# Optimization experiments

Hardware: AMD Instinct MI355X
Metric: run time of the kernel (lower is better)

Reference implementation:

```python
import jax, jax.numpy as jnp
import numpy as np

B, D, K, DM = 4096, 64, 64, 512  # batch, latent_dim, num_charts, d_model
BALL_EPS = 1e-5


def _l2n(x):
    return x / (jnp.linalg.norm(x) + 1e-12)


def _spectral_scale(W, iters=5):
    # torch.nn.utils.spectral_norm semantics: power iteration with no-grad u,v,
    # gradient flows through W in sigma = u^T W v.
    Wd = jax.lax.stop_gradient(W)
    u = _l2n(jnp.ones((W.shape[0],), W.dtype))
    v = _l2n(Wd.T @ u)
    for _ in range(iters):
        v = _l2n(Wd.T @ u)
        u = _l2n(Wd @ v)
    sigma = u @ (W @ v)
    return W / sigma


def spectral_linear(x, W, b):
    return x @ _spectral_scale(W).T + b


def _project_to_ball(x):
    n = jnp.linalg.norm(x, axis=-1, keepdims=True)
    scale = jnp.minimum(1.0, (1.0 - BALL_EPS) / jnp.maximum(n, 1e-12))
    return x * scale


def _poincare_dist2(x, y):
    # x: [B, D] query positions, y: [B, K, D] chart centers -> squared geodesic dist [B, K]
    diff2 = jnp.sum((x[:, None, :] - y) ** 2, axis=-1)
    den = (1.0 - jnp.sum(x * x, axis=-1, keepdims=True)) * (1.0 - jnp.sum(y * y, axis=-1))
    arg = 1.0 + 2.0 * diff2 / jnp.maximum(den, 1e-12)
    d = jnp.arccosh(jnp.maximum(arg, 1.0 + 1e-7))
    return d * d


def covariant_attention(z_q, z_kv, x_q, x_k, x_v, Wq, bq, Wk, bk, Wv, bv, Wo, bo, geo_scale):
    # Single-head geodesic-biased attention (GeodesicConfig n_heads=1).
    q = x_q @ Wq.T + bq                               # [B, DM]
    k = jnp.einsum('bkd,ed->bke', x_k, Wk) + bk       # [B, K, DM]
    v = jnp.einsum('bkd,ed->bke', x_v, Wv) + bv       # [B, K, DM]
    scores = jnp.einsum('bd,bkd->bk', q, k) / jnp.sqrt(jnp.asarray(DM, q.dtype))
    scores = scores - geo_scale * _poincare_dist2(z_q, z_kv)
    attn = jax.nn.softmax(scores, axis=-1)            # [B, K]
    feat = jnp.einsum('bk,bkd->bd', attn, v)
    out = feat @ Wo.T + bo                            # [B, DM]
    return out, attn


def setup_inputs() -> dict:
    keys = jax.random.split(jax.random.key(0), 20)
    z = 0.05 * jax.random.normal(keys[0], (B, D), jnp.float32)      # inside unit ball
    rw = jax.nn.softmax(jax.random.normal(keys[1], (B, K), jnp.float32), axis=-1)
    chart_emb = 0.02 * jax.random.normal(keys[2], (K, DM), jnp.float32)
    cc = jax.random.normal(keys[3], (K, D), jnp.float32)
    chart_centers = 0.3 * (cc / jnp.linalg.norm(cc, axis=-1, keepdims=True))
    s = 0.02
    return {
        'z': z, 'rw': rw,
        'chart_emb': chart_emb, 'chart_centers': chart_centers,
        'zW': s * jax.random.normal(keys[4], (DM, D), jnp.float32),
        'zb': jnp.zeros((DM,), jnp.float32),
        'Wq': s * jax.random.normal(keys[5], (DM, DM), jnp.float32),
        'bq': jnp.zeros((DM,), jnp.float32),
        'Wk': s * jax.random.normal(keys[6], (DM, DM), jnp.float32),
        'bk': jnp.zeros((DM,), jnp.float32),
        'Wv': s * jax.random.normal(keys[7], (DM, DM), jnp.float32),
        'bv': jnp.zeros((DM,), jnp.float32),
        'Wo': s * jax.random.normal(keys[8], (DM, DM), jnp.float32),
        'bo': jnp.zeros((DM,), jnp.float32),
        'geo_scale': jnp.ones((), jnp.float32),
        'vW': s * jax.random.normal(keys[9], (1, DM), jnp.float32),
        'vb': jnp.zeros((1,), jnp.float32),
    }


def reference(z, rw, chart_emb, chart_centers, zW, zb, Wq, bq, Wk, bk, Wv, bv, Wo, bo, geo_scale, vW, vb):
    # ChartTokenizer: broadcast-multiply router weights with chart embeddings
    tokens_x = rw[:, :, None] * chart_emb[None]            # [B, K, DM]
    tokens_z = jnp.broadcast_to(_project_to_ball(chart_centers)[None], (z.shape[0], K, D))
    # z embedding (SpectralLinear)
    x_q = spectral_linear(z, zW, zb)                       # [B, DM]
    # critic covariant attention
    v_feat, _ = covariant_attention(z, tokens_z, x_q, tokens_x, tokens_x,
                                    Wq, bq, Wk, bk, Wv, bv, Wo, bo, geo_scale)
    # task value head (SpectralLinear -> scalar)
    return spectral_linear(v_feat, vW, vb)                 # [B, 1]
```

## Files before the change

### kernel.cpp

```cpp
#include <hip/hip_runtime.h>
#include <math.h>

#define WS_INV    0
#define WS_INVSV  1
#define WS_BOVW   2
#define WS_BVWO   3
#define WS_N2V    4
#define WS_COLSUM 64
#define WS_A      128
#define WS_WO0    4224
#define WS_QZB    4736
#define WS_CK0    5248
#define WS_CVW    5312
#define WS_NY2    5376
#define WS_YT     5440
#define WS_T1     16384
#define WS_V1     49152
#define WS_P1     81920
#define WS_GP     114688

#define PRE_LDSB  (36928 * 4)
#define MID_LDSB  (8192 * 4)
#define MAIN_LDSB (8448 * 4)

__device__ __forceinline__ float wave_sum(float x) {
#pragma unroll
    for (int o = 32; o; o >>= 1) x += __shfl_xor(x, o);
    return x;
}

__device__ __forceinline__ float block_sum512(float v, float* red) {
    float s = wave_sum(v);
    const int wid = threadIdx.x >> 6;
    __syncthreads();
    if ((threadIdx.x & 63) == 0) red[wid] = s;
    __syncthreads();
    float t2 = 0.0f;
#pragma unroll
    for (int i = 0; i < 8; ++i) t2 += red[i];
    return t2;
}

__global__ __launch_bounds__(512) void k_pre(
    const float* __restrict__ zW, const float* __restrict__ zb,
    const float* __restrict__ Wq, const float* __restrict__ bq,
    const float* __restrict__ Wk, const float* __restrict__ Wv,
    const float* __restrict__ Wo, const float* __restrict__ ce,
    const float* __restrict__ cc, const float* __restrict__ vW,
    const float* __restrict__ bo, float* __restrict__ ws)
{
    extern __shared__ float sm[];
    const int blk = blockIdx.x, t = threadIdx.x;
    const int lane = t & 63, w = t >> 6;

    if (blk < 128) {
        const int f0 = blk * 4;
        float* ces = sm;
        float* wkv = sm + 32832;
        {
            const float4* ce4 = (const float4*)ce;
#pragma unroll 4
            for (int i = 0; i < 16; ++i) {
                const int idx4 = i * 512 + t;
                const int k = idx4 >> 7, c4 = idx4 & 127;
                const float4 v = ce4[idx4];
                float* dst = &ces[k * 513 + c4 * 4];
                dst[0] = v.x; dst[1] = v.y; dst[2] = v.z; dst[3] = v.w;
            }
        }
        {
            const float4* Wk4 = (const float4*)Wk;
            const float4* Wv4 = (const float4*)Wv;
            float4* wkv4 = (float4*)wkv;
#pragma unroll
            for (int i = 0; i < 2; ++i) {
                const int idx = i * 512 + t;
                const int a = idx >> 7, c4 = idx & 127;
                wkv4[idx] = (a < 4) ? Wk4[(f0 + a) * 128 + c4]
                                    : Wv4[(f0 + a - 4) * 128 + c4];
            }
        }
        __syncthreads();
        float acc[8];
#pragma unroll
        for (int a = 0; a < 8; ++a) acc[a] = 0.0f;
        const int c0 = w * 64;
#pragma unroll 2
        for (int q4 = 0; q4 < 16; ++q4) {
            const int c = c0 + q4 * 4;
            const float cv0 = ces[lane * 513 + c + 0];
            const float cv1 = ces[lane * 513 + c + 1];
            const float cv2 = ces[lane * 513 + c + 2];
            const float cv3 = ces[lane * 513 + c + 3];
#pragma unroll
            for (int a = 0; a < 8; ++a) {
                const float4 wv4 = *(const float4*)&wkv[a * 512 + c];
                acc[a] = fmaf(wv4.x, cv0, acc[a]);
                acc[a] = fmaf(wv4.y, cv1, acc[a]);
                acc[a] = fmaf(wv4.z, cv2, acc[a]);
                acc[a] = fmaf(wv4.w, cv3, acc[a]);
            }
        }
        __syncthreads();
        float* part = sm;
#pragma unroll
        for (int a = 0; a < 8; ++a) part[(a * 8 + w) * 65 + lane] = acc[a];
        __syncthreads();
        {
            float s = 0.0f;
#pragma unroll
            for (int ww = 0; ww < 8; ++ww) s += part[(w * 8 + ww) * 65 + lane];
            if (w < 4) ws[WS_T1 + (f0 + w) * 64 + lane] = s;
            else       ws[WS_V1 + (f0 + w - 4) * 64 + lane] = s;
        }

    } else if (blk < 192) {
        const int f0 = (blk - 128) * 8;
        float* zl = sm;
        float* wq = sm + 32768;
        {
            const float4* zW4 = (const float4*)zW;
            float4* zl4 = (float4*)zl;
#pragma unroll 4
            for (int i = 0; i < 16; ++i) zl4[i * 512 + t] = zW4[i * 512 + t];
            const float4* Wq4 = (const float4*)Wq;
            float4* wq4 = (float4*)wq;
#pragma unroll
            for (int i = 0; i < 2; ++i)
                wq4[i * 512 + t] = Wq4[f0 * 128 + i * 512 + t];
        }
        __syncthreads();
        float acc[8];
#pragma unroll
        for (int a = 0; a < 8; ++a) acc[a] = 0.0f;
        const int e0 = w * 64;
#pragma unroll 2
        for (int q4 = 0; q4 < 16; ++q4) {
            const int e = e0 + q4 * 4;
            const float z0 = zl[(e + 0) * 64 + lane];
            const float z1 = zl[(e + 1) * 64 + lane];
            const float z2 = zl[(e + 2) * 64 + lane];
            const float z3 = zl[(e + 3) * 64 + lane];
#pragma unroll
            for (int fi = 0; fi < 8; ++fi) {
                const float4 q4v = *(const float4*)&wq[fi * 512 + e];
                acc[fi] = fmaf(q4v.x, z0, acc[fi]);
                acc[fi] = fmaf(q4v.y, z1, acc[fi]);
                acc[fi] = fmaf(q4v.z, z2, acc[fi]);
                acc[fi] = fmaf(q4v.w, z3, acc[fi]);
            }
        }
        __syncthreads();
        float* part = sm;
#pragma unroll
        for (int a = 0; a < 8; ++a) part[(a * 8 + w) * 65 + lane] = acc[a];
        __syncthreads();
        {
            float s = 0.0f;
#pragma unroll
            for (int ww = 0; ww < 8; ++ww) s += part[(w * 8 + ww) * 65 + lane];
            ws[WS_P1 + (f0 + w) * 64 + lane] = s;
        }

    } else if (blk < 200) {
        const int r0 = (blk - 192) * 8;
        float* zl = sm;
        {
            const float4* zW4 = (const float4*)zW;
            float4* zl4 = (float4*)zl;
#pragma unroll 4
            for (int i = 0; i < 16; ++i) zl4[i * 512 + t] = zW4[i * 512 + t];
        }
        __syncthreads();
        float acc[8];
#pragma unroll
        for (int a = 0; a < 8; ++a) acc[a] = 0.0f;
        float cs = 0.0f;
        const int e0 = w * 64;
#pragma unroll 2
        for (int q4 = 0; q4 < 16; ++q4) {
            const int e = e0 + q4 * 4;
#pragma unroll
            for (int j = 0; j < 4; ++j) {
                const float zv = zl[(e + j) * 64 + lane];
                cs += zv;
                const float4 b0 = *(const float4*)&zl[(e + j) * 64 + r0];
                const float4 b1 = *(const float4*)&zl[(e + j) * 64 + r0 + 4];
                acc[0] = fmaf(b0.x, zv, acc[0]);
                acc[1] = fmaf(b0.y, zv, acc[1]);
                acc[2] = fmaf(b0.z, zv, acc[2]);
                acc[3] = fmaf(b0.w, zv, acc[3]);
                acc[4] = fmaf(b1.x, zv, acc[4]);
                acc[5] = fmaf(b1.y, zv, acc[5]);
                acc[6] = fmaf(b1.z, zv, acc[6]);
                acc[7] = fmaf(b1.w, zv, acc[7]);
            }
        }
        __syncthreads();
        float* part = sm;
        float* part2 = sm + 4160;
#pragma unroll
        for (int a = 0; a < 8; ++a) part[(a * 8 + w) * 65 + lane] = acc[a];
        if (blk == 192) part2[w * 65 + lane] = cs;
        __syncthreads();
        {
            float s = 0.0f;
#pragma unroll
            for (int ww = 0; ww < 8; ++ww) s += part[(w * 8 + ww) * 65 + lane];
            ws[WS_A + (r0 + w) * 64 + lane] = s;
        }
        if (blk == 192 && t < 64) {
            float s = 0.0f;
#pragma unroll
            for (int ww = 0; ww < 8; ++ww) s += part2[ww * 65 + t];
            ws[WS_COLSUM + t] = s;
        }

    } else if (blk < 208) {
        const int f0 = (blk - 200) * 64;
        float zbr[8];
#pragma unroll
        for (int i = 0; i < 8; ++i) zbr[i] = zb[i * 64 + lane];
#pragma unroll
        for (int ff = 0; ff < 8; ++ff) {
            const int f = f0 + w * 8 + ff;
            float s = 0.0f;
#pragma unroll
            for (int i = 0; i < 8; ++i)
                s = fmaf(Wq[f * 512 + i * 64 + lane], zbr[i], s);
            s = wave_sum(s);
            if (lane == 0) ws[WS_QZB + f] = s + bq[f];
        }

    } else if (blk < 216) {
        const int e0 = (blk - 208) * 64;
        float s = 0.0f;
#pragma unroll 4
        for (int gi = 0; gi < 64; ++gi) {
            const int g = w * 64 + gi;
            s = fmaf(Wo[g * 512 + e0 + lane], vW[g], s);
        }
        float* part = sm;
        part[w * 65 + lane] = s;
        __syncthreads();
        if (t < 64) {
            float o = 0.0f;
#pragma unroll
            for (int ww = 0; ww < 8; ++ww) o += part[ww * 65 + t];
            ws[WS_WO0 + e0 + t] = o;
        }

    } else {
        float* red = sm;
        const float vwt = vW[t];
        const float n2v = block_sum512(vwt * vwt, red);
        if (t == 0) ws[WS_N2V] = n2v;
        const float bv_ = block_sum512(bo[t] * vwt, red);
        if (t == 0) ws[WS_BOVW] = bv_;
        if (t < 64) {
            float n2 = 0.0f;
            for (int dd = 0; dd < 64; ++dd) {
                const float c = cc[t * 64 + dd];
                n2 = fmaf(c, c, n2);
            }
            const float n = sqrtf(n2);
            const float scale = fminf(1.0f, (1.0f - 1e-5f) / fmaxf(n, 1e-12f));
            float s2 = 0.0f;
            for (int dd = 0; dd < 64; ++dd) {
                const float yv = cc[t * 64 + dd] * scale;
                ws[WS_YT + dd * 64 + t] = yv;
                s2 = fmaf(yv, yv, s2);
            }
            ws[WS_NY2 + t] = s2;
        }
    }
}

__global__ __launch_bounds__(512) void k_mid(
    const float* __restrict__ bv, float* __restrict__ ws)
{
    extern __shared__ float sm[];
    const int blk = blockIdx.x, t = threadIdx.x;
    const int lane = t & 63, w = t >> 6;

    if (blk == 0) {
        float* As = sm;
        float* wL = sm + 4160;
        float* mvL = sm + 4224;
#pragma unroll
        for (int i = 0; i < 8; ++i) {
            const int idx = i * 512 + t;
            As[(idx >> 6) * 65 + (idx & 63)] = ws[WS_A + idx];
        }
        if (t < 64) wL[t] = ws[WS_COLSUM + t];
        __syncthreads();
        const int row = t >> 3, sub = t & 7;
#pragma unroll
        for (int it = 0; it < 4; ++it) {
            float p = 0.0f;
#pragma unroll
            for (int j = 0; j < 8; ++j)
                p = fmaf(As[row * 65 + sub * 8 + j], wL[sub * 8 + j], p);
            p += __shfl_xor(p, 1);
            p += __shfl_xor(p, 2);
            p += __shfl_xor(p, 4);
            __syncthreads();
            if (sub == 0) wL[row] = p;
            __syncthreads();
        }
        {
            float p = 0.0f;
#pragma unroll
            for (int j = 0; j < 8; ++j)
                p = fmaf(As[row * 65 + sub * 8 + j], wL[sub * 8 + j], p);
            p += __shfl_xor(p, 1);
            p += __shfl_xor(p, 2);
            p += __shfl_xor(p, 4);
            if (sub == 0) mvL[row] = p;
            __syncthreads();
        }
        if (w == 0) {
            const float w4 = wL[lane], mv = mvL[lane];
            const float s8 = wave_sum(w4 * w4);
            const float s9 = wave_sum(mv * w4);
            const float den = sqrtf(s8) + 1e-12f;
            const float n5sq = s9 / (den * den);
            const float n5 = sqrtf(n5sq);
            const float sig = n5sq / (n5 + 1e-12f);
            if (lane == 0) ws[WS_INV] = 1.0f / sig;
        } else if (w == 1) {
            float s = 0.0f;
#pragma unroll
            for (int i = 0; i < 8; ++i)
                s = fmaf(bv[i * 64 + lane], ws[WS_WO0 + i * 64 + lane], s);
            s = wave_sum(s);
            if (lane == 0) ws[WS_BVWO] = s;
        } else if (w == 2 && lane == 0) {
            const float n2 = ws[WS_N2V];
            const float rn = sqrtf(n2);
            float u = 1.0f / (1.0f + 1e-12f), s = 0.0f;
            for (int it = 0; it < 5; ++it) {
                const float nv = fabsf(u) * rn;
                const float vs = u / (nv + 1e-12f);
                s = n2 * vs;
                u = s / (fabsf(s) + 1e-12f);
            }
            ws[WS_INVSV] = 1.0f / (u * s);
        }

    } else if (blk < 3) {
        const int mat = (blk == 1) ? WS_V1 : WS_T1;
        const int vec = (blk == 1) ? WS_WO0 : WS_QZB;
        const int dst = (blk == 1) ? WS_CVW : WS_CK0;
        float s = 0.0f;
#pragma unroll 4
        for (int i = 0; i < 64; ++i) {
            const int e = w * 64 + i;
            s = fmaf(ws[mat + e * 64 + lane], ws[vec + e], s);
        }
        float* part = sm;
        part[w * 65 + lane] = s;
        __syncthreads();
        if (t < 64) {
            float o = 0.0f;
#pragma unroll
            for (int ww = 0; ww < 8; ++ww) o += part[ww * 65 + t];
            ws[dst + t] = o;
        }

    } else {
        const int p = blk - 3;
        const int f0 = p * 64;
        float* T1s = sm;
        float* P1s = sm + 4096;
        {
            const float4* a4 = (const float4*)&ws[WS_T1 + f0 * 64];
            const float4* b4 = (const float4*)&ws[WS_P1 + f0 * 64];
            float4* T14 = (float4*)T1s;
            float4* P14 = (float4*)P1s;
#pragma unroll
            for (int i = 0; i < 2; ++i) {
                T14[i * 512 + t] = a4[i * 512 + t];
                P14[i * 512 + t] = b4[i * 512 + t];
            }
        }
        __syncthreads();
        float acc[8];
#pragma unroll
        for (int j = 0; j < 8; ++j) acc[j] = 0.0f;
        const int d0 = w * 8;
#pragma unroll 2
        for (int f = 0; f < 64; ++f) {
            const float a = T1s[f * 64 + lane];
            const float4 p0 = *(const float4*)&P1s[f * 64 + d0];
            const float4 p1 = *(const float4*)&P1s[f * 64 + d0 + 4];
            acc[0] = fmaf(a, p0.x, acc[0]);
            acc[1] = fmaf(a, p0.y, acc[1]);
            acc[2] = fmaf(a, p0.z, acc[2]);
            acc[3] = fmaf(a, p0.w, acc[3]);
            acc[4] = fmaf(a, p1.x, acc[4]);
            acc[5] = fmaf(a, p1.y, acc[5]);
            acc[6] = fmaf(a, p1.z, acc[6]);
            acc[7] = fmaf(a, p1.w, acc[7]);
        }
#pragma unroll
        for (int j = 0; j < 8; ++j)
            ws[WS_GP + p * 4096 + (d0 + j) * 64 + lane] = acc[j];
    }
}

__global__ __launch_bounds__(512) void k_main(
    const float* __restrict__ z, const float* __restrict__ rw,
    const float* __restrict__ geo, const float* __restrict__ vb,
    const float* __restrict__ ws, float* __restrict__ out)
{
    extern __shared__ float sm[];
    float* sGt  = sm;
    float* sYt  = sm + 4096;
    float* sCvw = sm + 8192;
    float* sCk0 = sm + 8256;
    float* sNy2 = sm + 8320;
    float* sSc  = sm + 8384;
    const int t = threadIdx.x;
    const int lane = t & 63, w = t >> 6;
    const float inv_s = ws[WS_INV];
    const float inv_sv = ws[WS_INVSV];
    {
        const float4* yt4 = (const float4*)(ws + WS_YT);
        float4* sGt4 = (float4*)sGt;
        float4* sYt4 = (float4*)sYt;
#pragma unroll
        for (int i = 0; i < 2; ++i) {
            const int i4 = i * 512 + t;
            float4 g0 = *(const float4*)(ws + WS_GP + i4 * 4);
#pragma unroll
            for (int p = 1; p < 8; ++p) {
                const float4 gp = *(const float4*)(ws + WS_GP + p * 4096 + i4 * 4);
                g0.x += gp.x; g0.y += gp.y; g0.z += gp.z; g0.w += gp.w;
            }
            g0.x *= inv_s; g0.y *= inv_s; g0.z *= inv_s; g0.w *= inv_s;
            sGt4[i4] = g0;
            sYt4[i4] = yt4[i4];
        }
    }
    if (t < 64) {
        sCvw[t] = inv_sv * ws[WS_CVW + t];
        sCk0[t] = ws[WS_CK0 + t];
        sNy2[t] = ws[WS_NY2 + t];
    }
    if (t == 0) {
        sSc[0] = inv_sv * (ws[WS_BVWO] + ws[WS_BOVW]) + vb[0];
        sSc[1] = geo[0];
    }
    __syncthreads();
    const float gs = sSc[1], cst = sSc[0];
    const float rs512 = 0.04419417382415922f;
#pragma unroll
    for (int rr = 0; rr < 4; ++rr) {
        const int b = blockIdx.x * 32 + w * 4 + rr;
        const float zl = z[b * 64 + lane];
        const float rwk = rw[b * 64 + lane];
        float dot = 0.0f, diff2 = 0.0f, nz2 = 0.0f;
#pragma unroll 8
        for (int dd = 0; dd < 64; ++dd) {
            const float zd = __shfl(zl, dd);
            nz2 = fmaf(zd, zd, nz2);
            dot = fmaf(zd, sGt[dd * 64 + lane], dot);
            const float df = zd - sYt[dd * 64 + lane];
            diff2 = fmaf(df, df, diff2);
        }
        const float den = (1.0f - nz2) * (1.0f - sNy2[lane]);
        float arg = 1.0f + 2.0f * diff2 / fmaxf(den, 1e-12f);
        arg = fmaxf(arg, 1.0f + 1e-7f);
        const float dg = acoshf(arg);
        const float score = rwk * (dot + sCk0[lane]) * rs512 - gs * dg * dg;
        float mx = score;
#pragma unroll
        for (int o = 32; o; o >>= 1) mx = fmaxf(mx, __shfl_xor(mx, o));
        const float e = expf(score - mx);
        float s1 = e, s2 = e * rwk * sCvw[lane];
#pragma unroll
        for (int o = 32; o; o >>= 1) { s1 += __shfl_xor(s1, o); s2 += __shfl_xor(s2, o); }
        if (lane == 0) out[b] = s2 / s1 + cst;
    }
}

extern "C" void kernel_launch(void* const* d_in, const int* in_sizes, int n_in,
                              void* d_out, int out_size, void* d_ws, size_t ws_size,
                              hipStream_t stream)
{
    (void)in_sizes; (void)n_in; (void)out_size; (void)ws_size;
    const float* z   = (const float*)d_in[0];
    const float* rw  = (const float*)d_in[1];
    const float* cem = (const float*)d_in[2];
    const float* cc  = (const float*)d_in[3];
    const float* zW  = (const float*)d_in[4];
    const float* zb  = (const float*)d_in[5];
    const float* Wq  = (const float*)d_in[6];
    const float* bq  = (const float*)d_in[7];
    const float* Wk  = (const float*)d_in[8];
    const float* Wv  = (const float*)d_in[10];
    const float* bv  = (const float*)d_in[11];
    const float* Wo  = (const float*)d_in[12];
    const float* bo  = (const float*)d_in[13];
    const float* geo = (const float*)d_in[14];
    const float* vW  = (const float*)d_in[15];
    const float* vb  = (const float*)d_in[16];
    float* ws  = (float*)d_ws;
    float* out = (float*)d_out;

    hipLaunchKernelGGL(k_pre,  dim3(217), dim3(512), PRE_LDSB, stream,
                       zW, zb, Wq, bq, Wk, Wv, Wo, cem, cc, vW, bo, ws);
    hipLaunchKernelGGL(k_mid,  dim3(11),  dim3(512), MID_LDSB, stream, bv, ws);
    hipLaunchKernelGGL(k_main, dim3(128), dim3(512), MAIN_LDSB, stream,
                       z, rw, geo, vb, ws, out);
}
```

Before: 34.48 us.

## Reduce G partials in last k_mid block, recompute ball projection in k_main, smaller blocks

The last finishing block of k_mid, chosen with an atomic counter, now reduces the 8 G partial sums into a single matrix. k_main therefore reads one matrix instead of 8 partials per block. The chart-center ball projection moves from a single serial thread group in k_pre into each k_main block, computed in parallel with float4 loads and shuffles. k_main now runs 256 blocks of 256 threads with static LDS, and the Y layout is padded to stride 65. The changes trade redundant per-block projection work and an atomic/fence step against a shorter serial tail in k_pre and less global traffic in k_main.

```diff
diff --git a/kernel.cpp b/kernel.cpp
--- a/kernel.cpp
+++ b/kernel.cpp
@@ -6,22 +6,21 @@
 #define WS_BOVW   2
 #define WS_BVWO   3
 #define WS_N2V    4
+#define WS_CNT_I  6
 #define WS_COLSUM 64
 #define WS_A      128
 #define WS_WO0    4224
 #define WS_QZB    4736
 #define WS_CK0    5248
 #define WS_CVW    5312
-#define WS_NY2    5376
-#define WS_YT     5440
 #define WS_T1     16384
 #define WS_V1     49152
 #define WS_P1     81920
 #define WS_GP     114688
+#define WS_GT     147456
 
 #define PRE_LDSB  (36928 * 4)
 #define MID_LDSB  (8192 * 4)
-#define MAIN_LDSB (8448 * 4)
 
 __device__ __forceinline__ float wave_sum(float x) {
 #pragma unroll
@@ -46,8 +45,8 @@
     const float* __restrict__ Wq, const float* __restrict__ bq,
     const float* __restrict__ Wk, const float* __restrict__ Wv,
     const float* __restrict__ Wo, const float* __restrict__ ce,
-    const float* __restrict__ cc, const float* __restrict__ vW,
-    const float* __restrict__ bo, float* __restrict__ ws)
+    const float* __restrict__ vW, const float* __restrict__ bo,
+    float* __restrict__ ws)
 {
     extern __shared__ float sm[];
     const int blk = blockIdx.x, t = threadIdx.x;
@@ -256,22 +255,9 @@
         const float n2v = block_sum512(vwt * vwt, red);
         if (t == 0) ws[WS_N2V] = n2v;
         const float bv_ = block_sum512(bo[t] * vwt, red);
-        if (t == 0) ws[WS_BOVW] = bv_;
-        if (t < 64) {
-            float n2 = 0.0f;
-            for (int dd = 0; dd < 64; ++dd) {
-                const float c = cc[t * 64 + dd];
-                n2 = fmaf(c, c, n2);
-            }
-            const float n = sqrtf(n2);
-            const float scale = fminf(1.0f, (1.0f - 1e-5f) / fmaxf(n, 1e-12f));
-            float s2 = 0.0f;
-            for (int dd = 0; dd < 64; ++dd) {
-                const float yv = cc[t * 64 + dd] * scale;
-                ws[WS_YT + dd * 64 + t] = yv;
-                s2 = fmaf(yv, yv, s2);
-            }
-            ws[WS_NY2 + t] = s2;
+        if (t == 0) {
+            ws[WS_BOVW] = bv_;
+            ((int*)ws)[WS_CNT_I] = 0;
         }
     }
 }
@@ -280,6 +266,7 @@
     const float* __restrict__ bv, float* __restrict__ ws)
 {
     extern __shared__ float sm[];
+    __shared__ int isLast;
     const int blk = blockIdx.x, t = threadIdx.x;
     const int lane = t & 63, w = t >> 6;
 
@@ -353,7 +340,7 @@
         const int vec = (blk == 1) ? WS_WO0 : WS_QZB;
         const int dst = (blk == 1) ? WS_CVW : WS_CK0;
         float s = 0.0f;
-#pragma unroll 4
+#pragma unroll 8
         for (int i = 0; i < 64; ++i) {
             const int e = w * 64 + i;
             s = fmaf(ws[mat + e * 64 + lane], ws[vec + e], s);
@@ -406,58 +393,106 @@
 #pragma unroll
         for (int j = 0; j < 8; ++j)
             ws[WS_GP + p * 4096 + (d0 + j) * 64 + lane] = acc[j];
+
+        __syncthreads();
+        if (t == 0) {
+            __threadfence();
+            const int old = __hip_atomic_fetch_add((int*)ws + WS_CNT_I, 1,
+                                                   __ATOMIC_ACQ_REL,
+                                                   __HIP_MEMORY_SCOPE_AGENT);
+            isLast = (old == 7);
+        }
+        __syncthreads();
+        if (isLast) {
+            __threadfence();
+#pragma unroll
+            for (int i = 0; i < 2; ++i) {
+                const int i4 = i * 512 + t;
+                float4 g = *(const float4*)(ws + WS_GP + i4 * 4);
+#pragma unroll
+                for (int q = 1; q < 8; ++q) {
+                    const float4 gp = *(const float4*)(ws + WS_GP + q * 4096 + i4 * 4);
+                    g.x += gp.x; g.y += gp.y; g.z += gp.z; g.w += gp.w;
+                }
+                *(float4*)(ws + WS_GT + i4 * 4) = g;
+            }
+        }
     }
 }
 
-__global__ __launch_bounds__(512) void k_main(
+__global__ __launch_bounds__(256) void k_main(
     const float* __restrict__ z, const float* __restrict__ rw,
     const float* __restrict__ geo, const float* __restrict__ vb,
-    const float* __restrict__ ws, float* __restrict__ out)
+    const float* __restrict__ cc, const float* __restrict__ ws,
+    float* __restrict__ out)
 {
-    extern __shared__ float sm[];
-    float* sGt  = sm;
-    float* sYt  = sm + 4096;
-    float* sCvw = sm + 8192;
-    float* sCk0 = sm + 8256;
-    float* sNy2 = sm + 8320;
-    float* sSc  = sm + 8384;
+    __shared__ float sGt[4096];
+    __shared__ float sYt[4160];
+    __shared__ float sCvw[64], sCk0[64], sNy2[64], sSc[2];
     const int t = threadIdx.x;
-    const int lane = t & 63, w = t >> 6;
+    const int lane = t & 63, wid = t >> 6;
     const float inv_s = ws[WS_INV];
     const float inv_sv = ws[WS_INVSV];
+
     {
-        const float4* yt4 = (const float4*)(ws + WS_YT);
         float4* sGt4 = (float4*)sGt;
-        float4* sYt4 = (float4*)sYt;
-#pragma unroll
-        for (int i = 0; i < 2; ++i) {
-            const int i4 = i * 512 + t;
-            float4 g0 = *(const float4*)(ws + WS_GP + i4 * 4);
-#pragma unroll
-            for (int p = 1; p < 8; ++p) {
-                const float4 gp = *(const float4*)(ws + WS_GP + p * 4096 + i4 * 4);
-                g0.x += gp.x; g0.y += gp.y; g0.z += gp.z; g0.w += gp.w;
-            }
-            g0.x *= inv_s; g0.y *= inv_s; g0.z *= inv_s; g0.w *= inv_s;
-            sGt4[i4] = g0;
-            sYt4[i4] = yt4[i4];
-        }
+#pragma unroll
+        for (int i = 0; i < 4; ++i) {
+            const int i4 = i * 256 + t;
+            float4 g = *(const float4*)(ws + WS_GT + i4 * 4);
+            g.x *= inv_s; g.y *= inv_s; g.z *= inv_s; g.w *= inv_s;
+            sGt4[i4] = g;
+        }
+    }
+    {
+        const int k = t >> 2, q = t & 3;
+        const float4* cc4 = (const float4*)cc;
+        float4 v[4];
+        float n2 = 0.0f;
+#pragma unroll
+        for (int j = 0; j < 4; ++j) {
+            v[j] = cc4[k * 16 + q * 4 + j];
+            n2 = fmaf(v[j].x, v[j].x, n2);
+            n2 = fmaf(v[j].y, v[j].y, n2);
+            n2 = fmaf(v[j].z, v[j].z, n2);
+            n2 = fmaf(v[j].w, v[j].w, n2);
+        }
+        n2 += __shfl_xor(n2, 1);
+        n2 += __shfl_xor(n2, 2);
+        const float n = sqrtf(n2);
+        const float scale = fminf(1.0f, (1.0f - 1e-5f) / fmaxf(n, 1e-12f));
+        float s2 = 0.0f;
+#pragma unroll
+        for (int j = 0; j < 4; ++j) {
+            const float y0 = v[j].x * scale, y1 = v[j].y * scale;
+            const float y2 = v[j].z * scale, y3 = v[j].w * scale;
+            const int dd = q * 16 + j * 4;
+            sYt[(dd + 0) * 65 + k] = y0;
+            sYt[(dd + 1) * 65 + k] = y1;
+            sYt[(dd + 2) * 65 + k] = y2;
+            sYt[(dd + 3) * 65 + k] = y3;
+            s2 = fmaf(y0, y0, s2); s2 = fmaf(y1, y1, s2);
+            s2 = fmaf(y2, y2, s2); s2 = fmaf(y3, y3, s2);
+        }
+        s2 += __shfl_xor(s2, 1);
+        s2 += __shfl_xor(s2, 2);
+        if (q == 0) sNy2[k] = s2;
     }
     if (t < 64) {
         sCvw[t] = inv_sv * ws[WS_CVW + t];
         sCk0[t] = ws[WS_CK0 + t];
-        sNy2[t] = ws[WS_NY2 + t];
     }
     if (t == 0) {
         sSc[0] = inv_sv * (ws[WS_BVWO] + ws[WS_BOVW]) + vb[0];
         sSc[1] = geo[0];
     }
     __syncthreads();
+
     const float gs = sSc[1], cst = sSc[0];
     const float rs512 = 0.04419417382415922f;
 #pragma unroll
     for (int rr = 0; rr < 4; ++rr) {
-        const int b = blockIdx.x * 32 + w * 4 + rr;
+        const int b = blockIdx.x * 16 + wid * 4 + rr;
         const float zl = z[b * 64 + lane];
         const float rwk = rw[b * 64 + lane];
         float dot = 0.0f, diff2 = 0.0f, nz2 = 0.0f;
@@ -466,7 +501,7 @@
             const float zd = __shfl(zl, dd);
             nz2 = fmaf(zd, zd, nz2);
             dot = fmaf(zd, sGt[dd * 64 + lane], dot);
-            const float df = zd - sYt[dd * 64 + lane];
+            const float df = zd - sYt[dd * 65 + lane];
             diff2 = fmaf(df, df, diff2);
         }
         const float den = (1.0f - nz2) * (1.0f - sNy2[lane]);
@@ -510,8 +545,8 @@
     float* out = (float*)d_out;
 
     hipLaunchKernelGGL(k_pre,  dim3(217), dim3(512), PRE_LDSB, stream,
-                       zW, zb, Wq, bq, Wk, Wv, Wo, cem, cc, vW, bo, ws);
+                       zW, zb, Wq, bq, Wk, Wv, Wo, cem, vW, bo, ws);
     hipLaunchKernelGGL(k_mid,  dim3(11),  dim3(512), MID_LDSB, stream, bv, ws);
-    hipLaunchKernelGGL(k_main, dim3(128), dim3(512), MAIN_LDSB, stream,
-                       z, rw, geo, vb, ws, out);
+    hipLaunchKernelGGL(k_main, dim3(256), dim3(256), 0, stream,
+                       z, rw, geo, vb, cc, ws, out);
 }
```

Result: slower. 59.24 us (+71.8%).
